# Kernel optimization log

Measured on AMD Instinct MI355X. Metric: run time of the kernel, lower is better.

Reference implementation:

```python
import jax, jax.numpy as jnp
import numpy as np

IN_FEATURES = 2048
OUT_FEATURES = 2048
BATCH = 32768
EPS = 1e-10

def setup_inputs() -> dict:
    key = jax.random.key(0)
    kx, kp = jax.random.split(key)
    x = jax.random.normal(kx, (BATCH, IN_FEATURES), dtype=jnp.float32)
    P = jax.random.normal(kp, (OUT_FEATURES, IN_FEATURES), dtype=jnp.float32)
    bias = jnp.zeros((OUT_FEATURES,), dtype=jnp.float32)
    return {"x": x, "P": P, "bias": bias}

def reference(x, P, bias):
    # Gram matrix of columns of P: [in, in]
    PTP = jnp.abs(P.T @ P)
    # per-column (dim=0 sum) AOL rescaling factor: [in]
    d = 1.0 / jnp.sqrt(PTP.sum(axis=0) + EPS)
    # W = P @ diag(d) == column-wise scale of P
    W = P * d[None, :]          # [out, in]
    return x @ W.T + bias        # [batch, out]
```

## Files before the change

kernel.cpp:

```cpp
#include <hip/hip_runtime.h>
#include <hip/hip_bf16.h>
#include <stdint.h>

#define IN_F  2048
#define OUT_F 2048
#define BATCH 32768

typedef __attribute__((ext_vector_type(8))) short  short8;
typedef __attribute__((ext_vector_type(4))) float  floatx4;

#define GLD16(g, l) __builtin_amdgcn_global_load_lds( \
    (const __attribute__((address_space(1))) void*)(g), \
    (__attribute__((address_space(3))) void*)(l), 16, 0, 0)

__device__ __forceinline__ uint16_t f2bf(float f) {
  union { float f; uint32_t u; } v; v.f = f;
  uint32_t r = v.u + 0x7FFFu + ((v.u >> 16) & 1u);
  return (uint16_t)(r >> 16);
}

__global__ __launch_bounds__(256) void k_transpose_bf16(
    const float* __restrict__ P, uint16_t* __restrict__ PT) {
  __shared__ float tile[32][33];
  const int bx = blockIdx.x * 32;
  const int by = blockIdx.y * 32;
  const int tx = threadIdx.x & 31;
  const int ty = threadIdx.x >> 5;
#pragma unroll
  for (int i = 0; i < 32; i += 8)
    tile[ty + i][tx] = P[(size_t)(by + ty + i) * IN_F + bx + tx];
  __syncthreads();
#pragma unroll
  for (int i = 0; i < 32; i += 8)
    PT[(size_t)(bx + ty + i) * IN_F + by + tx] = f2bf(tile[tx][ty + i]);
}

__global__ __launch_bounds__(256) void k_gram_colsum(
    const uint16_t* __restrict__ PT, float* __restrict__ colsum) {
  __shared__ __align__(16) uint16_t lA[128 * 32];
  __shared__ __align__(16) uint16_t lB[128 * 32];
  __shared__ float colpart[128];

  const int tid = threadIdx.x;
  const int wave = tid >> 6, lane = tid & 63;
  const int bm = blockIdx.x * 128, bn = blockIdx.y * 128;
  const int wm = (wave >> 1) * 64, wn = (wave & 1) * 64;

  floatx4 z = {0.f, 0.f, 0.f, 0.f};
  floatx4 acc[4][4];
#pragma unroll
  for (int i = 0; i < 4; i++)
#pragma unroll
    for (int j = 0; j < 4; j++) acc[i][j] = z;

  const int srow = wave * 32 + (lane >> 2);
  const int scol = (lane & 3) * 8;
  const uint16_t* gA0 = PT + (size_t)(bm + srow) * IN_F + scol;
  const uint16_t* gA1 = gA0 + 16 * IN_F;
  const uint16_t* gB0 = PT + (size_t)(bn + srow) * IN_F + scol;
  const uint16_t* gB1 = gB0 + 16 * IN_F;
  uint16_t* lA0 = &lA[wave * 1024]; uint16_t* lA1 = lA0 + 512;
  uint16_t* lB0 = &lB[wave * 1024]; uint16_t* lB1 = lB0 + 512;

  const int la = (wm + (lane & 15)) * 32 + (lane >> 4) * 8;
  const int lb = (wn + (lane & 15)) * 32 + (lane >> 4) * 8;

  for (int k0 = 0; k0 < IN_F; k0 += 32) {
    GLD16(gA0, lA0); GLD16(gA1, lA1);
    GLD16(gB0, lB0); GLD16(gB1, lB1);
    gA0 += 32; gA1 += 32; gB0 += 32; gB1 += 32;
    __syncthreads();
    short8 af[4], bf[4];
#pragma unroll
    for (int i = 0; i < 4; i++) {
      af[i] = *(const short8*)&lA[la + i * 512];
      bf[i] = *(const short8*)&lB[lb + i * 512];
    }
#pragma unroll
    for (int i = 0; i < 4; i++)
#pragma unroll
      for (int j = 0; j < 4; j++)
        acc[i][j] = __builtin_amdgcn_mfma_f32_16x16x32_bf16(af[i], bf[j], acc[i][j], 0, 0, 0);
    __syncthreads();
  }

  if (tid < 128) colpart[tid] = 0.f;
  __syncthreads();
#pragma unroll
  for (int j = 0; j < 4; j++) {
    float s = 0.f;
#pragma unroll
    for (int i = 0; i < 4; i++)
#pragma unroll
      for (int r = 0; r < 4; r++) s += fabsf(acc[i][j][r]);
    atomicAdd(&colpart[wn + j * 16 + (lane & 15)], s);
  }
  __syncthreads();
  if (tid < 128) atomicAdd(&colsum[bn + tid], colpart[tid]);
}

__global__ void k_finalize_d(const float* __restrict__ colsum, float* __restrict__ dv) {
  int i = blockIdx.x * blockDim.x + threadIdx.x;
  if (i < IN_F) dv[i] = 1.0f / sqrtf(colsum[i] + 1e-10f);
}

__global__ __launch_bounds__(256) void k_scale_p(
    const float4* __restrict__ P4, const float4* __restrict__ dv4,
    uint2* __restrict__ WB) {
  int t = blockIdx.x * 256 + threadIdx.x;
  int col4 = t & (IN_F / 4 - 1);
  float4 p = P4[t];
  float4 d = dv4[col4];
  uint2 o;
  o.x = (uint32_t)f2bf(p.x * d.x) | ((uint32_t)f2bf(p.y * d.y) << 16);
  o.y = (uint32_t)f2bf(p.z * d.z) | ((uint32_t)f2bf(p.w * d.w) << 16);
  WB[t] = o;
}

__global__ __launch_bounds__(256) void k_cvt_x(
    const float4* __restrict__ X4, uint4* __restrict__ XB) {
  size_t t = (size_t)blockIdx.x * 256 + threadIdx.x;
  float4 a = X4[2 * t], b = X4[2 * t + 1];
  uint4 o;
  o.x = (uint32_t)f2bf(a.x) | ((uint32_t)f2bf(a.y) << 16);
  o.y = (uint32_t)f2bf(a.z) | ((uint32_t)f2bf(a.w) << 16);
  o.z = (uint32_t)f2bf(b.x) | ((uint32_t)f2bf(b.y) << 16);
  o.w = (uint32_t)f2bf(b.z) | ((uint32_t)f2bf(b.w) << 16);
  XB[t] = o;
}

__global__ __launch_bounds__(256) void k_gemm_nt(
    const uint16_t* __restrict__ A,
    const uint16_t* __restrict__ B,
    const float* __restrict__ bias,
    float* __restrict__ C) {
  __shared__ __align__(16) uint16_t lA[128 * 32];
  __shared__ __align__(16) uint16_t lB[128 * 32];

  const int tid = threadIdx.x;
  const int wave = tid >> 6, lane = tid & 63;
  const int bm = blockIdx.x * 128;
  const int bn = blockIdx.y * 128;
  const int wm = (wave >> 1) * 64, wn = (wave & 1) * 64;

  floatx4 z = {0.f, 0.f, 0.f, 0.f};
  floatx4 acc[4][4];
#pragma unroll
  for (int i = 0; i < 4; i++)
#pragma unroll
    for (int j = 0; j < 4; j++) acc[i][j] = z;

  const int srow = wave * 32 + (lane >> 2);
  const int scol = (lane & 3) * 8;
  const uint16_t* gA0 = A + (size_t)(bm + srow) * IN_F + scol;
  const uint16_t* gA1 = gA0 + 16 * IN_F;
  const uint16_t* gB0 = B + (size_t)(bn + srow) * IN_F + scol;
  const uint16_t* gB1 = gB0 + 16 * IN_F;
  uint16_t* lA0 = &lA[wave * 1024]; uint16_t* lA1 = lA0 + 512;
  uint16_t* lB0 = &lB[wave * 1024]; uint16_t* lB1 = lB0 + 512;

  const int la = (wm + (lane & 15)) * 32 + (lane >> 4) * 8;
  const int lb = (wn + (lane & 15)) * 32 + (lane >> 4) * 8;

  for (int k0 = 0; k0 < IN_F; k0 += 32) {
    GLD16(gA0, lA0); GLD16(gA1, lA1);
    GLD16(gB0, lB0); GLD16(gB1, lB1);
    gA0 += 32; gA1 += 32; gB0 += 32; gB1 += 32;
    __syncthreads();
    short8 af[4], bf[4];
#pragma unroll
    for (int i = 0; i < 4; i++) {
      af[i] = *(const short8*)&lA[la + i * 512];
      bf[i] = *(const short8*)&lB[lb + i * 512];
    }
#pragma unroll
    for (int i = 0; i < 4; i++)
#pragma unroll
      for (int j = 0; j < 4; j++)
        acc[i][j] = __builtin_amdgcn_mfma_f32_16x16x32_bf16(af[i], bf[j], acc[i][j], 0, 0, 0);
    __syncthreads();
  }

#pragma unroll
  for (int j = 0; j < 4; j++) {
    const int col = bn + wn + j * 16 + (lane & 15);
    const float bv = bias[col];
#pragma unroll
    for (int i = 0; i < 4; i++) {
      const int row0 = bm + wm + i * 16 + (lane >> 4) * 4;
#pragma unroll
      for (int r = 0; r < 4; r++)
        C[(size_t)(row0 + r) * OUT_F + col] = acc[i][j][r] + bv;
    }
  }
}

__global__ __launch_bounds__(256) void fb_gram(const float* __restrict__ P,
                                               float* __restrict__ colsum) {
  __shared__ float red[256];
  const int j = blockIdx.x;
  float s = 0.f;
  for (int i = threadIdx.x; i < IN_F; i += 256) {
    float dot = 0.f;
    for (int k = 0; k < OUT_F; k++)
      dot = fmaf(P[(size_t)k * IN_F + i], P[(size_t)k * IN_F + j], dot);
    s += fabsf(dot);
  }
  red[threadIdx.x] = s;
  __syncthreads();
  for (int st = 128; st > 0; st >>= 1) {
    if (threadIdx.x < st) red[threadIdx.x] += red[threadIdx.x + st];
    __syncthreads();
  }
  if (threadIdx.x == 0) colsum[j] = red[0];
}

__global__ __launch_bounds__(256) void fb_gemm(
    const float* __restrict__ X, const float* __restrict__ P,
    const float* __restrict__ dv, const float* __restrict__ bias,
    float* __restrict__ out) {
  __shared__ __align__(16) float xs[64][20];
  __shared__ __align__(16) float ps[64][20];
  const int bm = blockIdx.x * 64, bn = blockIdx.y * 64;
  const int tx = threadIdx.x & 15, ty = threadIdx.x >> 4;
  float acc[4][4] = {};
  const int r = threadIdx.x >> 2, kc = (threadIdx.x & 3) * 4;
  for (int k0 = 0; k0 < IN_F; k0 += 16) {
    float4 xv = *(const float4*)&X[(size_t)(bm + r) * IN_F + k0 + kc];
    float4 pv = *(const float4*)&P[(size_t)(bn + r) * IN_F + k0 + kc];
    float4 dd = *(const float4*)&dv[k0 + kc];
    float4 pw; pw.x = pv.x * dd.x; pw.y = pv.y * dd.y; pw.z = pv.z * dd.z; pw.w = pv.w * dd.w;
    *(float4*)&xs[r][kc] = xv;
    *(float4*)&ps[r][kc] = pw;
    __syncthreads();
#pragma unroll
    for (int kk = 0; kk < 16; kk++) {
      float a0[4], b0[4];
#pragma unroll
      for (int i = 0; i < 4; i++) a0[i] = xs[ty * 4 + i][kk];
#pragma unroll
      for (int jj = 0; jj < 4; jj++) b0[jj] = ps[tx * 4 + jj][kk];
#pragma unroll
      for (int i = 0; i < 4; i++)
#pragma unroll
        for (int jj = 0; jj < 4; jj++) acc[i][jj] = fmaf(a0[i], b0[jj], acc[i][jj]);
    }
    __syncthreads();
  }
#pragma unroll
  for (int i = 0; i < 4; i++)
#pragma unroll
    for (int jj = 0; jj < 4; jj++) {
      int row = bm + ty * 4 + i, col = bn + tx * 4 + jj;
      out[(size_t)row * OUT_F + col] = acc[i][jj] + bias[col];
    }
}

extern "C" void kernel_launch(void* const* d_in, const int* in_sizes, int n_in,
                              void* d_out, int out_size, void* d_ws, size_t ws_size,
                              hipStream_t stream) {
  const float* x    = (const float*)d_in[0];
  const float* P    = (const float*)d_in[1];
  const float* bias = (const float*)d_in[2];
  float* out = (float*)d_out;
  char* ws = (char*)d_ws;

  const size_t SZ_PT = (size_t)IN_F * OUT_F * 2;
  const size_t SZ_WB = (size_t)IN_F * OUT_F * 2;
  const size_t SZ_XB = (size_t)BATCH * IN_F * 2;
  const size_t need  = SZ_PT + SZ_WB + SZ_XB + 2 * IN_F * sizeof(float) + 256;

  if (ws_size >= need) {
    uint16_t* PT = (uint16_t*)ws;
    uint16_t* WB = (uint16_t*)(ws + SZ_PT);
    uint16_t* XB = (uint16_t*)(ws + SZ_PT + SZ_WB);
    float* colsum = (float*)(ws + SZ_PT + SZ_WB + SZ_XB);
    float* dv = colsum + IN_F;

    hipMemsetAsync(colsum, 0, IN_F * sizeof(float), stream);
    k_transpose_bf16<<<dim3(64, 64), 256, 0, stream>>>(P, PT);
    k_gram_colsum<<<dim3(16, 16), 256, 0, stream>>>(PT, colsum);
    k_finalize_d<<<8, 256, 0, stream>>>(colsum, dv);
    k_scale_p<<<(IN_F * OUT_F / 4) / 256, 256, 0, stream>>>(
        (const float4*)P, (const float4*)dv, (uint2*)WB);
    k_cvt_x<<<(int)(((size_t)BATCH * IN_F / 8) / 256), 256, 0, stream>>>(
        (const float4*)x, (uint4*)XB);
    k_gemm_nt<<<dim3(BATCH / 128, OUT_F / 128), 256, 0, stream>>>(XB, WB, bias, out);
  } else {
    float* colsum = (float*)ws;
    float* dv = colsum + IN_F;
    fb_gram<<<IN_F, 256, 0, stream>>>(P, colsum);
    k_finalize_d<<<8, 256, 0, stream>>>(colsum, dv);
    fb_gemm<<<dim3(BATCH / 64, OUT_F / 64), 256, 0, stream>>>(x, P, dv, bias, out);
  }
}
```

Baseline: 962.6 us.

## Double-buffer GEMM LDS tiles with padding and fold column scale into x conversion

Replaces the direct global-to-LDS loads in both GEMMs with a register-staged, double-buffered pipeline. LDS rows are padded to 40 elements to avoid bank conflicts, and one barrier per k-step replaces two, so global loads overlap the MFMA work. The d scaling moves from P onto x during bf16 conversion, and the prep kernel writes bf16 P alongside the transpose, which removes the separate scale kernel. In exchange this doubles LDS use, which may lower occupancy, and it changes where bf16 rounding happens.

```diff
diff --git a/kernel.cpp b/kernel.cpp
--- a/kernel.cpp
+++ b/kernel.cpp
@@ -9,9 +9,7 @@
 typedef __attribute__((ext_vector_type(8))) short  short8;
 typedef __attribute__((ext_vector_type(4))) float  floatx4;
 
-#define GLD16(g, l) __builtin_amdgcn_global_load_lds( \
-    (const __attribute__((address_space(1))) void*)(g), \
-    (__attribute__((address_space(3))) void*)(l), 16, 0, 0)
+static constexpr int LDT = 40;
 
 __device__ __forceinline__ uint16_t f2bf(float f) {
   union { float f; uint32_t u; } v; v.f = f;
@@ -19,16 +17,81 @@
   return (uint16_t)(r >> 16);
 }
 
-__global__ __launch_bounds__(256) void k_transpose_bf16(
-    const float* __restrict__ P, uint16_t* __restrict__ PT) {
+__device__ __forceinline__ void gemm128_pipeline(
+    const uint16_t* __restrict__ A, const uint16_t* __restrict__ B,
+    int bm, int bn, int K, uint16_t* sA, uint16_t* sB,
+    floatx4 (&acc)[4][4]) {
+  const int tid  = threadIdx.x;
+  const int wave = tid >> 6, lane = tid & 63;
+  const int wm = (wave >> 1) * 64, wn = (wave & 1) * 64;
+
+  const int srow = wave * 32 + (lane >> 2);
+  const int scol = (lane & 3) * 8;
+  const uint16_t* gA = A + (size_t)(bm + srow) * K + scol;
+  const uint16_t* gB = B + (size_t)(bn + srow) * K + scol;
+
+  const int wAo  = srow * LDT + scol;
+  const int wAo2 = (srow + 16) * LDT + scol;
+
+  const int ra = (wm + (lane & 15)) * LDT + (lane >> 4) * 8;
+  const int rb = (wn + (lane & 15)) * LDT + (lane >> 4) * 8;
+
+  short8 rA0 = *(const short8*)gA;
+  short8 rA1 = *(const short8*)(gA + 16 * (size_t)K);
+  short8 rB0 = *(const short8*)gB;
+  short8 rB1 = *(const short8*)(gB + 16 * (size_t)K);
+  gA += 32; gB += 32;
+  *(short8*)&sA[wAo]  = rA0;  *(short8*)&sA[wAo2] = rA1;
+  *(short8*)&sB[wAo]  = rB0;  *(short8*)&sB[wAo2] = rB1;
+  __syncthreads();
+
+  const int NK = K / 32;
+  int p = 0;
+  for (int k = 0; k < NK; k++, p ^= 1) {
+    if (k + 1 < NK) {
+      rA0 = *(const short8*)gA;
+      rA1 = *(const short8*)(gA + 16 * (size_t)K);
+      rB0 = *(const short8*)gB;
+      rB1 = *(const short8*)(gB + 16 * (size_t)K);
+      gA += 32; gB += 32;
+    }
+    const uint16_t* cA = sA + p * (128 * LDT);
+    const uint16_t* cB = sB + p * (128 * LDT);
+    short8 af[4], bf[4];
+#pragma unroll
+    for (int i = 0; i < 4; i++) {
+      af[i] = *(const short8*)&cA[ra + i * 16 * LDT];
+      bf[i] = *(const short8*)&cB[rb + i * 16 * LDT];
+    }
+#pragma unroll
+    for (int i = 0; i < 4; i++)
+#pragma unroll
+      for (int j = 0; j < 4; j++)
+        acc[i][j] = __builtin_amdgcn_mfma_f32_16x16x32_bf16(af[i], bf[j], acc[i][j], 0, 0, 0);
+    if (k + 1 < NK) {
+      uint16_t* dA = sA + (p ^ 1) * (128 * LDT);
+      uint16_t* dB = sB + (p ^ 1) * (128 * LDT);
+      *(short8*)&dA[wAo]  = rA0;  *(short8*)&dA[wAo2] = rA1;
+      *(short8*)&dB[wAo]  = rB0;  *(short8*)&dB[wAo2] = rB1;
+    }
+    __syncthreads();
+  }
+}
+
+__global__ __launch_bounds__(256) void k_prep(
+    const float* __restrict__ P, uint16_t* __restrict__ PT,
+    uint16_t* __restrict__ PB) {
   __shared__ float tile[32][33];
   const int bx = blockIdx.x * 32;
   const int by = blockIdx.y * 32;
   const int tx = threadIdx.x & 31;
   const int ty = threadIdx.x >> 5;
 #pragma unroll
-  for (int i = 0; i < 32; i += 8)
-    tile[ty + i][tx] = P[(size_t)(by + ty + i) * IN_F + bx + tx];
+  for (int i = 0; i < 32; i += 8) {
+    float v = P[(size_t)(by + ty + i) * IN_F + bx + tx];
+    tile[ty + i][tx] = v;
+    PB[(size_t)(by + ty + i) * IN_F + bx + tx] = f2bf(v);
+  }
   __syncthreads();
 #pragma unroll
   for (int i = 0; i < 32; i += 8)
@@ -37,14 +100,14 @@
 
 __global__ __launch_bounds__(256) void k_gram_colsum(
     const uint16_t* __restrict__ PT, float* __restrict__ colsum) {
-  __shared__ __align__(16) uint16_t lA[128 * 32];
-  __shared__ __align__(16) uint16_t lB[128 * 32];
+  __shared__ __align__(16) uint16_t sA[2 * 128 * LDT];
+  __shared__ __align__(16) uint16_t sB[2 * 128 * LDT];
   __shared__ float colpart[128];
 
   const int tid = threadIdx.x;
   const int wave = tid >> 6, lane = tid & 63;
   const int bm = blockIdx.x * 128, bn = blockIdx.y * 128;
-  const int wm = (wave >> 1) * 64, wn = (wave & 1) * 64;
+  const int wn = (wave & 1) * 64;
 
   floatx4 z = {0.f, 0.f, 0.f, 0.f};
   floatx4 acc[4][4];
@@ -53,36 +116,7 @@
 #pragma unroll
     for (int j = 0; j < 4; j++) acc[i][j] = z;
 
-  const int srow = wave * 32 + (lane >> 2);
-  const int scol = (lane & 3) * 8;
-  const uint16_t* gA0 = PT + (size_t)(bm + srow) * IN_F + scol;
-  const uint16_t* gA1 = gA0 + 16 * IN_F;
-  const uint16_t* gB0 = PT + (size_t)(bn + srow) * IN_F + scol;
-  const uint16_t* gB1 = gB0 + 16 * IN_F;
-  uint16_t* lA0 = &lA[wave * 1024]; uint16_t* lA1 = lA0 + 512;
-  uint16_t* lB0 = &lB[wave * 1024]; uint16_t* lB1 = lB0 + 512;
-
-  const int la = (wm + (lane & 15)) * 32 + (lane >> 4) * 8;
-  const int lb = (wn + (lane & 15)) * 32 + (lane >> 4) * 8;
-
-  for (int k0 = 0; k0 < IN_F; k0 += 32) {
-    GLD16(gA0, lA0); GLD16(gA1, lA1);
-    GLD16(gB0, lB0); GLD16(gB1, lB1);
-    gA0 += 32; gA1 += 32; gB0 += 32; gB1 += 32;
-    __syncthreads();
-    short8 af[4], bf[4];
-#pragma unroll
-    for (int i = 0; i < 4; i++) {
-      af[i] = *(const short8*)&lA[la + i * 512];
-      bf[i] = *(const short8*)&lB[lb + i * 512];
-    }
-#pragma unroll
-    for (int i = 0; i < 4; i++)
-#pragma unroll
-      for (int j = 0; j < 4; j++)
-        acc[i][j] = __builtin_amdgcn_mfma_f32_16x16x32_bf16(af[i], bf[j], acc[i][j], 0, 0, 0);
-    __syncthreads();
-  }
+  gemm128_pipeline(PT, PT, bm, bn, OUT_F, sA, sB, acc);
 
   if (tid < 128) colpart[tid] = 0.f;
   __syncthreads();
@@ -104,28 +138,18 @@
   if (i < IN_F) dv[i] = 1.0f / sqrtf(colsum[i] + 1e-10f);
 }
 
-__global__ __launch_bounds__(256) void k_scale_p(
-    const float4* __restrict__ P4, const float4* __restrict__ dv4,
-    uint2* __restrict__ WB) {
-  int t = blockIdx.x * 256 + threadIdx.x;
-  int col4 = t & (IN_F / 4 - 1);
-  float4 p = P4[t];
-  float4 d = dv4[col4];
-  uint2 o;
-  o.x = (uint32_t)f2bf(p.x * d.x) | ((uint32_t)f2bf(p.y * d.y) << 16);
-  o.y = (uint32_t)f2bf(p.z * d.z) | ((uint32_t)f2bf(p.w * d.w) << 16);
-  WB[t] = o;
-}
-
 __global__ __launch_bounds__(256) void k_cvt_x(
-    const float4* __restrict__ X4, uint4* __restrict__ XB) {
+    const float4* __restrict__ X4, const float4* __restrict__ dv4,
+    uint4* __restrict__ XB) {
   size_t t = (size_t)blockIdx.x * 256 + threadIdx.x;
+  int c4 = (int)((2 * t) & (IN_F / 4 - 1));
   float4 a = X4[2 * t], b = X4[2 * t + 1];
+  float4 d0 = dv4[c4], d1 = dv4[c4 + 1];
   uint4 o;
-  o.x = (uint32_t)f2bf(a.x) | ((uint32_t)f2bf(a.y) << 16);
-  o.y = (uint32_t)f2bf(a.z) | ((uint32_t)f2bf(a.w) << 16);
-  o.z = (uint32_t)f2bf(b.x) | ((uint32_t)f2bf(b.y) << 16);
-  o.w = (uint32_t)f2bf(b.z) | ((uint32_t)f2bf(b.w) << 16);
+  o.x = (uint32_t)f2bf(a.x * d0.x) | ((uint32_t)f2bf(a.y * d0.y) << 16);
+  o.y = (uint32_t)f2bf(a.z * d0.z) | ((uint32_t)f2bf(a.w * d0.w) << 16);
+  o.z = (uint32_t)f2bf(b.x * d1.x) | ((uint32_t)f2bf(b.y * d1.y) << 16);
+  o.w = (uint32_t)f2bf(b.z * d1.z) | ((uint32_t)f2bf(b.w * d1.w) << 16);
   XB[t] = o;
 }
 
@@ -134,8 +158,8 @@
     const uint16_t* __restrict__ B,
     const float* __restrict__ bias,
     float* __restrict__ C) {
-  __shared__ __align__(16) uint16_t lA[128 * 32];
-  __shared__ __align__(16) uint16_t lB[128 * 32];
+  __shared__ __align__(16) uint16_t sA[2 * 128 * LDT];
+  __shared__ __align__(16) uint16_t sB[2 * 128 * LDT];
 
   const int tid = threadIdx.x;
   const int wave = tid >> 6, lane = tid & 63;
@@ -150,36 +174,7 @@
 #pragma unroll
     for (int j = 0; j < 4; j++) acc[i][j] = z;
 
-  const int srow = wave * 32 + (lane >> 2);
-  const int scol = (lane & 3) * 8;
-  const uint16_t* gA0 = A + (size_t)(bm + srow) * IN_F + scol;
-  const uint16_t* gA1 = gA0 + 16 * IN_F;
-  const uint16_t* gB0 = B + (size_t)(bn + srow) * IN_F + scol;
-  const uint16_t* gB1 = gB0 + 16 * IN_F;
-  uint16_t* lA0 = &lA[wave * 1024]; uint16_t* lA1 = lA0 + 512;
-  uint16_t* lB0 = &lB[wave * 1024]; uint16_t* lB1 = lB0 + 512;
-
-  const int la = (wm + (lane & 15)) * 32 + (lane >> 4) * 8;
-  const int lb = (wn + (lane & 15)) * 32 + (lane >> 4) * 8;
-
-  for (int k0 = 0; k0 < IN_F; k0 += 32) {
-    GLD16(gA0, lA0); GLD16(gA1, lA1);
-    GLD16(gB0, lB0); GLD16(gB1, lB1);
-    gA0 += 32; gA1 += 32; gB0 += 32; gB1 += 32;
-    __syncthreads();
-    short8 af[4], bf[4];
-#pragma unroll
-    for (int i = 0; i < 4; i++) {
-      af[i] = *(const short8*)&lA[la + i * 512];
-      bf[i] = *(const short8*)&lB[lb + i * 512];
-    }
-#pragma unroll
-    for (int i = 0; i < 4; i++)
-#pragma unroll
-      for (int j = 0; j < 4; j++)
-        acc[i][j] = __builtin_amdgcn_mfma_f32_16x16x32_bf16(af[i], bf[j], acc[i][j], 0, 0, 0);
-    __syncthreads();
-  }
+  gemm128_pipeline(A, B, bm, bn, IN_F, sA, sB, acc);
 
 #pragma unroll
   for (int j = 0; j < 4; j++) {
@@ -266,26 +261,24 @@
   char* ws = (char*)d_ws;
 
   const size_t SZ_PT = (size_t)IN_F * OUT_F * 2;
-  const size_t SZ_WB = (size_t)IN_F * OUT_F * 2;
+  const size_t SZ_PB = (size_t)IN_F * OUT_F * 2;
   const size_t SZ_XB = (size_t)BATCH * IN_F * 2;
-  const size_t need  = SZ_PT + SZ_WB + SZ_XB + 2 * IN_F * sizeof(float) + 256;
+  const size_t need  = SZ_PT + SZ_PB + SZ_XB + 2 * IN_F * sizeof(float) + 256;
 
   if (ws_size >= need) {
     uint16_t* PT = (uint16_t*)ws;
-    uint16_t* WB = (uint16_t*)(ws + SZ_PT);
-    uint16_t* XB = (uint16_t*)(ws + SZ_PT + SZ_WB);
-    float* colsum = (float*)(ws + SZ_PT + SZ_WB + SZ_XB);
+    uint16_t* PB = (uint16_t*)(ws + SZ_PT);
+    uint16_t* XB = (uint16_t*)(ws + SZ_PT + SZ_PB);
+    float* colsum = (float*)(ws + SZ_PT + SZ_PB + SZ_XB);
     float* dv = colsum + IN_F;
 
     hipMemsetAsync(colsum, 0, IN_F * sizeof(float), stream);
-    k_transpose_bf16<<<dim3(64, 64), 256, 0, stream>>>(P, PT);
+    k_prep<<<dim3(64, 64), 256, 0, stream>>>(P, PT, PB);
     k_gram_colsum<<<dim3(16, 16), 256, 0, stream>>>(PT, colsum);
     k_finalize_d<<<8, 256, 0, stream>>>(colsum, dv);
-    k_scale_p<<<(IN_F * OUT_F / 4) / 256, 256, 0, stream>>>(
-        (const float4*)P, (const float4*)dv, (uint2*)WB);
     k_cvt_x<<<(int)(((size_t)BATCH * IN_F / 8) / 256), 256, 0, stream>>>(
-        (const float4*)x, (uint4*)XB);
-    k_gemm_nt<<<dim3(BATCH / 128, OUT_F / 128), 256, 0, stream>>>(XB, WB, bias, out);
+        (const float4*)x, (const float4*)dv, (uint4*)XB);
+    k_gemm_nt<<<dim3(BATCH / 128, OUT_F / 128), 256, 0, stream>>>(XB, PB, bias, out);
   } else {
     float* colsum = (float*)ws;
     float* dv = colsum + IN_F;
```

New measurement: 878.7 us. 8.7% less time.
